# Performance work log

Hardware: AMD Instinct MI355X
Metric: run time of the kernel (lower is better)

Reference implementation:

```python
import math
import jax, jax.numpy as jnp
import numpy as np

B, S, D_MODEL, H = 8, 1024, 512, 8
HEAD = D_MODEL // H
MAX_REL = 16


def rel_index(length_q, length_k):
    # clipped relative-position index matrix [Lq, Lk] in [0, 2*MAX_REL]
    rq = jnp.arange(length_q)
    rk = jnp.arange(length_k)
    dist = rk[None, :] - rq[:, None]
    return jnp.clip(dist, -MAX_REL, MAX_REL) + MAX_REL


def setup_inputs() -> dict:
    key = jax.random.key(0)
    ks = jax.random.split(key, 13)
    sc = 1.0 / math.sqrt(D_MODEL)
    inp = {
        "query": jax.random.normal(ks[0], (B, S, D_MODEL), jnp.float32),
        "key": jax.random.normal(ks[1], (B, S, D_MODEL), jnp.float32),
        "value": jax.random.normal(ks[2], (B, S, D_MODEL), jnp.float32),
        "Wq": jax.random.normal(ks[3], (D_MODEL, D_MODEL), jnp.float32) * sc,
        "bq": jnp.zeros((D_MODEL,), jnp.float32),
        "Wk": jax.random.normal(ks[4], (D_MODEL, D_MODEL), jnp.float32) * sc,
        "bk": jnp.zeros((D_MODEL,), jnp.float32),
        "Wv": jax.random.normal(ks[5], (D_MODEL, D_MODEL), jnp.float32) * sc,
        "bv": jnp.zeros((D_MODEL,), jnp.float32),
        "Wo": jax.random.normal(ks[6], (D_MODEL, D_MODEL), jnp.float32) * sc,
        "bo": jnp.zeros((D_MODEL,), jnp.float32),
        "rel_k_table": jax.random.normal(ks[7], (2 * MAX_REL + 1, HEAD), jnp.float32),
        "rel_v_table": jax.random.normal(ks[8], (2 * MAX_REL + 1, HEAD), jnp.float32),
    }
    return inp


def reference(query, key, value, Wq, bq, Wk, bk, Wv, bv, Wo, bo, rel_k_table, rel_v_table):
    b, s, d = query.shape
    # input projections (torch Linear: x @ W.T + b)
    q = query @ Wq.T + bq  # [B,S,D]
    k = key @ Wk.T + bk
    v = value @ Wv.T + bv
    # split heads: [B,H,S,HEAD]
    qh = q.reshape(b, s, H, HEAD).transpose(0, 2, 1, 3)
    kh = k.reshape(b, s, H, HEAD).transpose(0, 2, 1, 3)
    vh = v.reshape(b, s, H, HEAD).transpose(0, 2, 1, 3)
    # content-content scores
    attn1 = jnp.einsum("bhqd,bhkd->bhqk", qh, kh)
    # content-position scores via gathered relative embeddings [S,S,HEAD]
    idx = rel_index(s, s)
    rk = rel_k_table[idx]
    attn2 = jnp.einsum("bhqd,qkd->bhqk", qh, rk)
    # NOTE: original code scales by sqrt(batch_size), reproduced faithfully
    scale = math.sqrt(float(B))
    attn = jax.nn.softmax((attn1 + attn2) / scale, axis=-1)
    # values: content + relative-position value term
    w1 = jnp.einsum("bhqk,bhkd->bhqd", attn, vh)
    rv = rel_v_table[idx]
    w2 = jnp.einsum("bhqk,qkd->bhqd", attn, rv)
    x = (w1 + w2).transpose(0, 2, 1, 3).reshape(b * s, d)
    return x @ Wo.T + bo
```

## Files before the change

kernel.cpp:

```cpp
#include <hip/hip_runtime.h>

typedef unsigned short u16;
typedef float f32x4 __attribute__((ext_vector_type(4)));
typedef __bf16 bf16x8 __attribute__((ext_vector_type(8)));

#define MFMA16(a, b, c) __builtin_amdgcn_mfma_f32_16x16x32_bf16((a), (b), (c), 0, 0, 0)

#define B_ 8
#define H_ 8
#define S_ 1024

__device__ __forceinline__ u16 f2bf(float f) {
  unsigned u = __float_as_uint(f);
  return (u16)((u + 0x7fffu + ((u >> 16) & 1u)) >> 16);
}
__device__ __forceinline__ unsigned cvtpk(float a, float b) {
  unsigned r;
  asm("v_cvt_pk_bf16_f32 %0, %1, %2" : "=v"(r) : "v"(a), "v"(b));
  return r;
}
__device__ __forceinline__ void gload16(const void* g, void* l) {
  __builtin_amdgcn_global_load_lds((__attribute__((address_space(1))) const void*)g,
                                   (__attribute__((address_space(3))) void*)l, 16, 0, 0);
}

__global__ void __launch_bounds__(256) convW(const float* __restrict__ s0, const float* __restrict__ s1,
                                             const float* __restrict__ s2, const float* __restrict__ s3,
                                             const float* __restrict__ s4,
                                             u16* __restrict__ d0, u16* __restrict__ d1, u16* __restrict__ d2,
                                             u16* __restrict__ d3, u16* __restrict__ d4) {
  size_t i = ((size_t)blockIdx.x * 256 + threadIdx.x) << 2;
  if (i >= 1050688) return;
  const float* s; u16* d; size_t off;
  if (i < 262144)       { s = s0; d = d0; off = i; }
  else if (i < 524288)  { s = s1; d = d1; off = i - 262144; }
  else if (i < 786432)  { s = s2; d = d2; off = i - 524288; }
  else if (i < 1048576) { s = s3; d = d3; off = i - 786432; }
  else                  { s = s4; d = d4; off = i - 1048576; }
  float4 f = *(const float4*)(s + off);
  uint2 o;
  o.x = cvtpk(f.x, f.y);
  o.y = cvtpk(f.z, f.w);
  *(uint2*)(d + off) = o;
}

__global__ void __launch_bounds__(512) qkv_gemm(const float* __restrict__ Aq, const float* __restrict__ Ak,
                                                const float* __restrict__ Av, const u16* __restrict__ Wqb,
                                                const u16* __restrict__ Wkb, const u16* __restrict__ Wvb,
                                                const float* __restrict__ bq, const float* __restrict__ bk,
                                                const float* __restrict__ bv, u16* __restrict__ Qh,
                                                u16* __restrict__ Kh, u16* __restrict__ Vt) {
  __shared__ float Asf[128 * 64];
  __shared__ u16 Bs[128 * 64];
  const int w = (blockIdx.x & 7) * 96 + (blockIdx.x >> 3);
  const int seg = w >> 8, bid = w & 255;
  const float* Af = seg == 0 ? Aq : (seg == 1 ? Ak : Av);
  const u16* W = seg == 0 ? Wqb : (seg == 1 ? Wkb : Wvb);
  const float* bias = seg == 0 ? bq : (seg == 1 ? bk : bv);
  const int tid = threadIdx.x, lane = tid & 63, wid = tid >> 6;
  const int c = lane & 15, g = lane >> 4;
  const int bm = bid >> 2, bn = bid & 3;
  const int m0 = bm << 7, n0 = bn << 7;
  const int wrow = (wid & 3) << 5;
  const int wcol = (wid >> 2) << 6;

  const f32x4 ZF = {0.f, 0.f, 0.f, 0.f};
  f32x4 acc[2][4];
#pragma unroll
  for (int i = 0; i < 2; ++i)
#pragma unroll
    for (int j = 0; j < 4; ++j) acc[i][j] = ZF;

  for (int kt = 0; kt < 512; kt += 64) {
    __syncthreads();
#pragma unroll
    for (int j = 0; j < 4; ++j) {
      int s0 = ((wid << 2) | j) << 6;
      int s = s0 + lane;
      int row = s >> 4;
      int colb_s = ((s & 15) << 4) ^ ((row & 7) << 4);
      gload16((const char*)Af + (((size_t)(m0 + row)) << 11) + (kt << 2) + colb_s,
              (char*)Asf + (s0 << 4));
    }
#pragma unroll
    for (int j = 0; j < 2; ++j) {
      int s0 = ((wid << 1) | j) << 6;
      int s = s0 + lane;
      int row = s >> 3;
      int off = ((s & 7) << 4) ^ ((row & 7) << 4);
      gload16((const char*)W + ((((size_t)(n0 + row)) << 9) + kt) * 2 + off,
              (char*)Bs + (s0 << 4));
    }
    __syncthreads();
#pragma unroll
    for (int kk = 0; kk < 2; ++kk) {
      bf16x8 af[2], bfr[4];
#pragma unroll
      for (int rt = 0; rt < 2; ++rt) {
        int row = wrow + (rt << 4) + c;
        int swz = (row & 7) << 4;
        const char* pA = (const char*)Asf + row * 256;
        int bb = (kk << 7) + (g << 5);
        float4 f0 = *(const float4*)(pA + (bb ^ swz));
        float4 f1 = *(const float4*)(pA + ((bb + 16) ^ swz));
        uint4 aw;
        aw.x = cvtpk(f0.x, f0.y); aw.y = cvtpk(f0.z, f0.w);
        aw.z = cvtpk(f1.x, f1.y); aw.w = cvtpk(f1.z, f1.w);
        af[rt] = __builtin_bit_cast(bf16x8, aw);
      }
#pragma unroll
      for (int ct = 0; ct < 4; ++ct) {
        int row = wcol + (ct << 4) + c;
        bfr[ct] = *(const bf16x8*)((const char*)Bs + row * 128 + (((kk << 6) | (g << 4)) ^ ((row & 7) << 4)));
      }
#pragma unroll
      for (int rt = 0; rt < 2; ++rt)
#pragma unroll
        for (int ct = 0; ct < 4; ++ct) acc[rt][ct] = MFMA16(af[rt], bfr[ct], acc[rt][ct]);
    }
  }

#pragma unroll
  for (int rt = 0; rt < 2; ++rt)
#pragma unroll
    for (int ct = 0; ct < 4; ++ct) {
      int n = n0 + wcol + (ct << 4) + c;
      float bv2 = bias[n];
      if (seg == 2) {
        int b2 = m0 >> 10;
        int sbase = (m0 & 1023) + wrow + (rt << 4) + (g << 2);
        int h2 = n >> 6, d2 = n & 63;
        uint2 o;
        o.x = cvtpk(acc[rt][ct][0] + bv2, acc[rt][ct][1] + bv2);
        o.y = cvtpk(acc[rt][ct][2] + bv2, acc[rt][ct][3] + bv2);
        *(uint2*)(Vt + ((((size_t)((b2 << 3) + h2) << 6) + d2) << 10) + sbase) = o;
      } else {
        u16* out = seg == 0 ? Qh : Kh;
#pragma unroll
        for (int r = 0; r < 4; ++r) {
          int m = m0 + wrow + (rt << 4) + (g << 2) + r;
          int b = m >> 10, s = m & 1023, h = n >> 6, d = n & 63;
          out[(((((size_t)(b * H_ + h)) << 10) + s) << 6) + d] = f2bf(acc[rt][ct][r] + bv2);
        }
      }
    }
}

__global__ void __launch_bounds__(512) gemm_out(const u16* __restrict__ A, const u16* __restrict__ W,
                                                const float* __restrict__ bias, float* __restrict__ out) {
  __shared__ u16 As[128 * 64];
  __shared__ u16 Bs[128 * 64];
  const int wb = (blockIdx.x & 7) * 32 + (blockIdx.x >> 3);
  const int tid = threadIdx.x, lane = tid & 63, wid = tid >> 6;
  const int c = lane & 15, g = lane >> 4;
  const int bm = wb >> 2, bn = wb & 3;
  const int m0 = bm << 7, n0 = bn << 7;
  const int wrow = (wid & 3) << 5;
  const int wcol = (wid >> 2) << 6;

  const f32x4 ZF = {0.f, 0.f, 0.f, 0.f};
  f32x4 acc[2][4];
#pragma unroll
  for (int i = 0; i < 2; ++i)
#pragma unroll
    for (int j = 0; j < 4; ++j) acc[i][j] = ZF;

  for (int kt = 0; kt < 512; kt += 64) {
    __syncthreads();
#pragma unroll
    for (int j = 0; j < 2; ++j) {
      int s0 = ((wid << 1) | j) << 6;
      int s = s0 + lane;
      int row = s >> 3;
      int off = ((s & 7) << 4) ^ ((row & 7) << 4);
      gload16((const char*)A + ((((size_t)(m0 + row)) << 9) + kt) * 2 + off, (char*)As + (s0 << 4));
      gload16((const char*)W + ((((size_t)(n0 + row)) << 9) + kt) * 2 + off, (char*)Bs + (s0 << 4));
    }
    __syncthreads();
#pragma unroll
    for (int kk = 0; kk < 2; ++kk) {
      bf16x8 af[2], bfr[4];
#pragma unroll
      for (int rt = 0; rt < 2; ++rt) {
        int row = wrow + (rt << 4) + c;
        af[rt] = *(const bf16x8*)((const char*)As + row * 128 + (((kk << 6) | (g << 4)) ^ ((row & 7) << 4)));
      }
#pragma unroll
      for (int ct = 0; ct < 4; ++ct) {
        int row = wcol + (ct << 4) + c;
        bfr[ct] = *(const bf16x8*)((const char*)Bs + row * 128 + (((kk << 6) | (g << 4)) ^ ((row & 7) << 4)));
      }
#pragma unroll
      for (int rt = 0; rt < 2; ++rt)
#pragma unroll
        for (int ct = 0; ct < 4; ++ct) acc[rt][ct] = MFMA16(af[rt], bfr[ct], acc[rt][ct]);
    }
  }

#pragma unroll
  for (int rt = 0; rt < 2; ++rt)
#pragma unroll
    for (int ct = 0; ct < 4; ++ct) {
      int n = n0 + wcol + (ct << 4) + c;
      float bv = bias[n];
#pragma unroll
      for (int r = 0; r < 4; ++r) {
        int m = m0 + wrow + (rt << 4) + (g << 2) + r;
        out[(((size_t)m) << 9) + n] = acc[rt][ct][r] + bv;
      }
    }
}

__global__ void __launch_bounds__(512) flash_kernel(const u16* __restrict__ Qh, const u16* __restrict__ Kh,
                                                    const u16* __restrict__ Vt, const u16* __restrict__ relkb,
                                                    const float* __restrict__ relv, u16* __restrict__ Xout) {
  __shared__ u16 Ks[2][64 * 64];
  __shared__ u16 Vs[2][64 * 64];
  __shared__ u16 Ps[128 * 64];
  __shared__ float qrelS[128 * 34];
  __shared__ u16 Pband[128 * 32];
  __shared__ float rv32S[64];

  const int tid = threadIdx.x, lane = tid & 63, wid = tid >> 6;
  const int c = lane & 15, g = lane >> 4;
  const int swz = ((blockIdx.x & 7) << 6) | (blockIdx.x >> 3);
  const int bh = swz >> 3, qt = swz & 7;
  const int qbase = qt << 7;
  const size_t rowbase = ((size_t)bh) << 10;
  const int qloc = (wid << 4) + c;
  const float K1 = 0.51013619f;
  const float C0 = 24.0f;

  bf16x8 qa[2];
  {
    const u16* qptr = Qh + ((rowbase + qbase + qloc) << 6);
    qa[0] = *(const bf16x8*)(qptr + (g << 3));
    qa[1] = *(const bf16x8*)(qptr + 32 + (g << 3));
  }

#define STAGE(buf, kt_) do { \
    const int k64_ = (kt_) << 6; \
    int L_ = (wid << 10) + lane * 16; \
    int row_ = L_ >> 7; \
    int off_ = (L_ & 127) ^ ((row_ & 7) << 4); \
    gload16((const char*)Kh + ((rowbase + k64_ + row_) << 7) + off_, (char*)Ks[buf] + (wid << 10)); \
    gload16((const char*)Vt + ((((size_t)bh << 6) + row_) << 11) + (k64_ << 1) + off_, (char*)Vs[buf] + (wid << 10)); \
  } while (0)

  STAGE(0, 0);

  ((uint4*)Pband)[tid] = uint4{0, 0, 0, 0};
  if (tid < 64) rv32S[tid] = relv[2048 + tid];

  {
    const f32x4 ZF = {0.f, 0.f, 0.f, 0.f};
#pragma unroll
    for (int t = 0; t < 3; ++t) {
      int rr = t * 16 + c; if (rr > 32) rr = 32;
      f32x4 qr = ZF;
#pragma unroll
      for (int kk = 0; kk < 2; ++kk) {
        bf16x8 ar = *(const bf16x8*)(relkb + (rr << 6) + (kk << 5) + (g << 3));
        qr = MFMA16(ar, qa[kk], qr);
      }
#pragma unroll
      for (int j = 0; j < 4; ++j) {
        int r = t * 16 + (g << 2) + j;
        if (r < 33) qrelS[qloc * 34 + r] = qr[j] * K1 - C0;
      }
    }
  }
  __syncthreads();

  const float bias_lo = qrelS[qloc * 34 + 0];
  const float bias_hi = qrelS[qloc * 34 + 32];

  int koff[4][2], voff[4][2], poffw[4];
#pragma unroll
  for (int t = 0; t < 4; ++t) {
#pragma unroll
    for (int kk = 0; kk < 2; ++kk)
      koff[t][kk] = ((t << 4) + c) * 128 + ((((kk << 6) | (g << 4))) ^ ((c & 7) << 4));
#pragma unroll
    for (int h2 = 0; h2 < 2; ++h2)
      voff[t][h2] = ((t << 4) + c) * 128 + ((((h2 << 6) | (g << 4))) ^ ((c & 7) << 4));
    poffw[t] = qloc * 128 + (((t << 5) | (g << 3)) ^ ((c & 7) << 4));
  }
  const int pr0 = qloc * 128 + ((g << 4) ^ ((c & 7) << 4));
  const int pr1 = pr0 ^ 64;

  const f32x4 ZF = {0.f, 0.f, 0.f, 0.f};
  f32x4 acc[4] = {ZF, ZF, ZF, ZF};
  float lsum = 0.f, lowsum = 0.f, psum = 0.f;

  for (int kt = 0; kt < 16; ++kt) {
    const int cur = kt & 1;
    if (kt < 15) STAGE(cur ^ 1, kt + 1);

    f32x4 sa[4];
#pragma unroll
    for (int t = 0; t < 4; ++t) {
      sa[t] = ZF;
#pragma unroll
      for (int kk = 0; kk < 2; ++kk) {
        bf16x8 bk = *(const bf16x8*)((const char*)Ks + (cur << 13) + koff[t][kk]);
        sa[t] = MFMA16(bk, qa[kk], sa[t]);
      }
    }

    const int D0 = (kt << 6) - qbase;
    float p[4][4];
    if (D0 >= 192) {
      float s = 0.f;
#pragma unroll
      for (int t = 0; t < 4; ++t)
#pragma unroll
        for (int j = 0; j < 4; ++j) {
          float pe = __builtin_amdgcn_exp2f(fmaf(sa[t][j], K1, bias_hi));
          p[t][j] = pe; s += pe;
        }
      lsum += s;
    } else if (D0 <= -128) {
      float s = 0.f;
#pragma unroll
      for (int t = 0; t < 4; ++t)
#pragma unroll
        for (int j = 0; j < 4; ++j) {
          float pe = __builtin_amdgcn_exp2f(fmaf(sa[t][j], K1, bias_lo));
          p[t][j] = pe; s += pe;
        }
      lsum += s; lowsum += s;
    } else {
#pragma unroll
      for (int t = 0; t < 4; ++t)
#pragma unroll
        for (int j = 0; j < 4; ++j) {
          int dlt = D0 + (t << 4) + (g << 2) + j - qloc;
          int idx = dlt < -16 ? 0 : (dlt > 16 ? 32 : dlt + 16);
          float pe = __builtin_amdgcn_exp2f(fmaf(sa[t][j], K1, qrelS[qloc * 34 + idx]));
          p[t][j] = pe;
          lsum += pe;
          if (dlt <= -16) lowsum += pe;
          else if (dlt < 16) { psum += pe; Pband[(qloc << 5) + dlt + 16] = f2bf(pe); }
        }
    }

#pragma unroll
    for (int t = 0; t < 4; ++t) {
      uint2 pk;
      pk.x = cvtpk(p[t][0], p[t][1]);
      pk.y = cvtpk(p[t][2], p[t][3]);
      *(uint2*)((char*)Ps + poffw[t]) = pk;
    }
    bf16x8 pb0 = *(const bf16x8*)((const char*)Ps + pr0);
    bf16x8 pb1 = *(const bf16x8*)((const char*)Ps + pr1);
#pragma unroll
    for (int dt = 0; dt < 4; ++dt) {
      bf16x8 av0 = *(const bf16x8*)((const char*)Vs + (cur << 13) + voff[dt][0]);
      bf16x8 av1 = *(const bf16x8*)((const char*)Vs + (cur << 13) + voff[dt][1]);
      acc[dt] = MFMA16(av0, pb0, acc[dt]);
      acc[dt] = MFMA16(av1, pb1, acc[dt]);
    }
    __syncthreads();
  }

  lsum += __shfl_xor(lsum, 16);   lsum += __shfl_xor(lsum, 32);
  lowsum += __shfl_xor(lowsum, 16); lowsum += __shfl_xor(lowsum, 32);
  psum += __shfl_xor(psum, 16);   psum += __shfl_xor(psum, 32);
  const float inv = 1.f / lsum;
  const float hsum = lsum - lowsum - psum;

  if (g == 0) Pband[qloc << 5] = f2bf(lowsum);

  u16* rvT = (u16*)qrelS;
  for (int i = tid; i < 4096; i += 512) rvT[i] = f2bf(relv[((i & 31) << 6) + (i >> 5)]);
  __syncthreads();

  bf16x8 pb2 = *(const bf16x8*)((const u16*)Pband + (qloc << 5) + (g << 3));
#pragma unroll
  for (int dt = 0; dt < 4; ++dt) {
    bf16x8 av = *(const bf16x8*)(rvT + (((dt << 4) + c) << 5) + (g << 3));
    acc[dt] = MFMA16(av, pb2, acc[dt]);
  }

  const int b = bh >> 3, h = bh & 7;
  const int q = qbase + qloc;
  u16* xb = Xout + ((((size_t)b << 10) + q) << 9) + (h << 6);
#pragma unroll
  for (int dt = 0; dt < 4; ++dt) {
    int d0 = (dt << 4) + (g << 2);
    float v0 = (acc[dt][0] + hsum * rv32S[d0 + 0]) * inv;
    float v1 = (acc[dt][1] + hsum * rv32S[d0 + 1]) * inv;
    float v2 = (acc[dt][2] + hsum * rv32S[d0 + 2]) * inv;
    float v3 = (acc[dt][3] + hsum * rv32S[d0 + 3]) * inv;
    uint2 o;
    o.x = cvtpk(v0, v1);
    o.y = cvtpk(v2, v3);
    *(uint2*)(xb + d0) = o;
  }
#undef STAGE
}

extern "C" void kernel_launch(void* const* d_in, const int* in_sizes, int n_in,
                              void* d_out, int out_size, void* d_ws, size_t ws_size,
                              hipStream_t stream) {
  (void)in_sizes; (void)n_in; (void)out_size; (void)ws_size;
  const float* query = (const float*)d_in[0];
  const float* key   = (const float*)d_in[1];
  const float* value = (const float*)d_in[2];
  const float* Wq = (const float*)d_in[3];
  const float* bq = (const float*)d_in[4];
  const float* Wk = (const float*)d_in[5];
  const float* bk = (const float*)d_in[6];
  const float* Wv = (const float*)d_in[7];
  const float* bv = (const float*)d_in[8];
  const float* Wo = (const float*)d_in[9];
  const float* bo = (const float*)d_in[10];
  const float* relk = (const float*)d_in[11];
  const float* relv = (const float*)d_in[12];

  char* ws = (char*)d_ws;
  u16*   Wqb   = (u16*)(ws + 25165824);
  u16*   Wkb   = (u16*)(ws + 25690112);
  u16*   Wvb   = (u16*)(ws + 26214400);
  u16*   Wob   = (u16*)(ws + 26738688);
  u16*   relkb = (u16*)(ws + 27262976);
  u16*   Qh    = (u16*)(ws + 27271168);
  u16*   Kh    = (u16*)(ws + 35659776);
  u16*   Vt    = (u16*)(ws + 52436992);
  u16*   Xout  = (u16*)(ws + 70262784);

  convW<<<1027, 256, 0, stream>>>(Wq, Wk, Wv, Wo, relk, Wqb, Wkb, Wvb, Wob, relkb);
  qkv_gemm<<<768, 512, 0, stream>>>(query, key, value, Wqb, Wkb, Wvb, bq, bk, bv, Qh, Kh, Vt);
  flash_kernel<<<512, 512, 0, stream>>>(Qh, Kh, Vt, relkb, relv, Xout);
  gemm_out<<<256, 512, 0, stream>>>(Xout, Wob, bo, (float*)d_out);
}
```

Measured before the change: 86.34 us.

## Double-buffer LDS staging in QKV and output projection GEMMs

Both projection GEMMs change from single-buffered 64-wide K tiles to double-buffered 32-wide K tiles. The next tile's global-to-LDS load is issued before the MFMAs on the current tile, so each iteration needs only one barrier. The aim is to hide global load latency behind compute. In exchange there are twice as many iterations and barriers, the swizzle is narrower (4-way on B), and LDS use stays the same.

```diff
diff --git a/kernel.cpp b/kernel.cpp
--- a/kernel.cpp
+++ b/kernel.cpp
@@ -50,8 +50,8 @@
                                                 const float* __restrict__ bq, const float* __restrict__ bk,
                                                 const float* __restrict__ bv, u16* __restrict__ Qh,
                                                 u16* __restrict__ Kh, u16* __restrict__ Vt) {
-  __shared__ float Asf[128 * 64];
-  __shared__ u16 Bs[128 * 64];
+  __shared__ float Asf[2][128 * 32];
+  __shared__ u16 Bs[2][128 * 32];
   const int w = (blockIdx.x & 7) * 96 + (blockIdx.x >> 3);
   const int seg = w >> 8, bid = w & 255;
   const float* Af = seg == 0 ? Aq : (seg == 1 ? Ak : Av);
@@ -64,6 +64,26 @@
   const int wrow = (wid & 3) << 5;
   const int wcol = (wid >> 2) << 6;
 
+#define STAGEQ(buf, kt_) do { \
+    _Pragma("unroll") \
+    for (int j_ = 0; j_ < 2; ++j_) { \
+      int s0_ = ((wid << 1) | j_) << 6; \
+      int s_ = s0_ + lane; \
+      int row_ = s_ >> 3; \
+      int sl_ = (s_ & 7) ^ (row_ & 7); \
+      gload16((const char*)Af + ((((size_t)(m0 + row_)) << 9) + (kt_)) * 4 + (sl_ << 4), \
+              (char*)Asf[buf] + (s0_ << 4)); \
+    } \
+    { \
+      int s0_ = wid << 6; \
+      int s_ = s0_ + lane; \
+      int row_ = s_ >> 2; \
+      int sl_ = (s_ & 3) ^ (row_ & 3); \
+      gload16((const char*)W + ((((size_t)(n0 + row_)) << 9) + (kt_)) * 2 + (sl_ << 4), \
+              (char*)Bs[buf] + (s0_ << 4)); \
+    } \
+  } while (0)
+
   const f32x4 ZF = {0.f, 0.f, 0.f, 0.f};
   f32x4 acc[2][4];
 #pragma unroll
@@ -71,53 +91,37 @@
 #pragma unroll
     for (int j = 0; j < 4; ++j) acc[i][j] = ZF;
 
-  for (int kt = 0; kt < 512; kt += 64) {
-    __syncthreads();
-#pragma unroll
-    for (int j = 0; j < 4; ++j) {
-      int s0 = ((wid << 2) | j) << 6;
-      int s = s0 + lane;
-      int row = s >> 4;
-      int colb_s = ((s & 15) << 4) ^ ((row & 7) << 4);
-      gload16((const char*)Af + (((size_t)(m0 + row)) << 11) + (kt << 2) + colb_s,
-              (char*)Asf + (s0 << 4));
-    }
-#pragma unroll
-    for (int j = 0; j < 2; ++j) {
-      int s0 = ((wid << 1) | j) << 6;
-      int s = s0 + lane;
-      int row = s >> 3;
-      int off = ((s & 7) << 4) ^ ((row & 7) << 4);
-      gload16((const char*)W + ((((size_t)(n0 + row)) << 9) + kt) * 2 + off,
-              (char*)Bs + (s0 << 4));
-    }
-    __syncthreads();
-#pragma unroll
-    for (int kk = 0; kk < 2; ++kk) {
-      bf16x8 af[2], bfr[4];
-#pragma unroll
-      for (int rt = 0; rt < 2; ++rt) {
-        int row = wrow + (rt << 4) + c;
-        int swz = (row & 7) << 4;
-        const char* pA = (const char*)Asf + row * 256;
-        int bb = (kk << 7) + (g << 5);
-        float4 f0 = *(const float4*)(pA + (bb ^ swz));
-        float4 f1 = *(const float4*)(pA + ((bb + 16) ^ swz));
-        uint4 aw;
-        aw.x = cvtpk(f0.x, f0.y); aw.y = cvtpk(f0.z, f0.w);
-        aw.z = cvtpk(f1.x, f1.y); aw.w = cvtpk(f1.z, f1.w);
-        af[rt] = __builtin_bit_cast(bf16x8, aw);
-      }
-#pragma unroll
-      for (int ct = 0; ct < 4; ++ct) {
-        int row = wcol + (ct << 4) + c;
-        bfr[ct] = *(const bf16x8*)((const char*)Bs + row * 128 + (((kk << 6) | (g << 4)) ^ ((row & 7) << 4)));
-      }
-#pragma unroll
-      for (int rt = 0; rt < 2; ++rt)
-#pragma unroll
-        for (int ct = 0; ct < 4; ++ct) acc[rt][ct] = MFMA16(af[rt], bfr[ct], acc[rt][ct]);
-    }
+  STAGEQ(0, 0);
+  __syncthreads();
+
+  for (int it = 0; it < 16; ++it) {
+    const int cur = it & 1;
+    if (it < 15) STAGEQ(cur ^ 1, (it + 1) << 5);
+
+    bf16x8 af[2], bfr[4];
+#pragma unroll
+    for (int rt = 0; rt < 2; ++rt) {
+      int row = wrow + (rt << 4) + c;
+      const char* pA = (const char*)Asf[cur] + row * 128;
+      int sw = row & 7;
+      float4 f0 = *(const float4*)(pA + ((((g << 1) | 0) ^ sw) << 4));
+      float4 f1 = *(const float4*)(pA + ((((g << 1) | 1) ^ sw) << 4));
+      uint4 aw;
+      aw.x = cvtpk(f0.x, f0.y); aw.y = cvtpk(f0.z, f0.w);
+      aw.z = cvtpk(f1.x, f1.y); aw.w = cvtpk(f1.z, f1.w);
+      af[rt] = __builtin_bit_cast(bf16x8, aw);
+    }
+#pragma unroll
+    for (int ct = 0; ct < 4; ++ct) {
+      int row = wcol + (ct << 4) + c;
+      bfr[ct] = *(const bf16x8*)((const char*)Bs[cur] + row * 64 + ((g ^ (row & 3)) << 4));
+    }
+#pragma unroll
+    for (int rt = 0; rt < 2; ++rt)
+#pragma unroll
+      for (int ct = 0; ct < 4; ++ct) acc[rt][ct] = MFMA16(af[rt], bfr[ct], acc[rt][ct]);
+
+    if (it < 15) __syncthreads();
   }
 
 #pragma unroll
@@ -144,12 +148,13 @@
         }
       }
     }
+#undef STAGEQ
 }
 
 __global__ void __launch_bounds__(512) gemm_out(const u16* __restrict__ A, const u16* __restrict__ W,
                                                 const float* __restrict__ bias, float* __restrict__ out) {
-  __shared__ u16 As[128 * 64];
-  __shared__ u16 Bs[128 * 64];
+  __shared__ u16 As2[2][128 * 32];
+  __shared__ u16 Bs2[2][128 * 32];
   const int wb = (blockIdx.x & 7) * 32 + (blockIdx.x >> 3);
   const int tid = threadIdx.x, lane = tid & 63, wid = tid >> 6;
   const int c = lane & 15, g = lane >> 4;
@@ -158,6 +163,17 @@
   const int wrow = (wid & 3) << 5;
   const int wcol = (wid >> 2) << 6;
 
+#define STAGEO(buf, kt_) do { \
+    int s0_ = wid << 6; \
+    int s_ = s0_ + lane; \
+    int row_ = s_ >> 2; \
+    int sl_ = (s_ & 3) ^ (row_ & 3); \
+    gload16((const char*)A + ((((size_t)(m0 + row_)) << 9) + (kt_)) * 2 + (sl_ << 4), \
+            (char*)As2[buf] + (s0_ << 4)); \
+    gload16((const char*)W + ((((size_t)(n0 + row_)) << 9) + (kt_)) * 2 + (sl_ << 4), \
+            (char*)Bs2[buf] + (s0_ << 4)); \
+  } while (0)
+
   const f32x4 ZF = {0.f, 0.f, 0.f, 0.f};
   f32x4 acc[2][4];
 #pragma unroll
@@ -165,36 +181,30 @@
 #pragma unroll
     for (int j = 0; j < 4; ++j) acc[i][j] = ZF;
 
-  for (int kt = 0; kt < 512; kt += 64) {
-    __syncthreads();
-#pragma unroll
-    for (int j = 0; j < 2; ++j) {
-      int s0 = ((wid << 1) | j) << 6;
-      int s = s0 + lane;
-      int row = s >> 3;
-      int off = ((s & 7) << 4) ^ ((row & 7) << 4);
-      gload16((const char*)A + ((((size_t)(m0 + row)) << 9) + kt) * 2 + off, (char*)As + (s0 << 4));
-      gload16((const char*)W + ((((size_t)(n0 + row)) << 9) + kt) * 2 + off, (char*)Bs + (s0 << 4));
-    }
-    __syncthreads();
-#pragma unroll
-    for (int kk = 0; kk < 2; ++kk) {
-      bf16x8 af[2], bfr[4];
-#pragma unroll
-      for (int rt = 0; rt < 2; ++rt) {
-        int row = wrow + (rt << 4) + c;
-        af[rt] = *(const bf16x8*)((const char*)As + row * 128 + (((kk << 6) | (g << 4)) ^ ((row & 7) << 4)));
-      }
-#pragma unroll
-      for (int ct = 0; ct < 4; ++ct) {
-        int row = wcol + (ct << 4) + c;
-        bfr[ct] = *(const bf16x8*)((const char*)Bs + row * 128 + (((kk << 6) | (g << 4)) ^ ((row & 7) << 4)));
-      }
-#pragma unroll
-      for (int rt = 0; rt < 2; ++rt)
-#pragma unroll
-        for (int ct = 0; ct < 4; ++ct) acc[rt][ct] = MFMA16(af[rt], bfr[ct], acc[rt][ct]);
-    }
+  STAGEO(0, 0);
+  __syncthreads();
+
+  for (int it = 0; it < 16; ++it) {
+    const int cur = it & 1;
+    if (it < 15) STAGEO(cur ^ 1, (it + 1) << 5);
+
+    bf16x8 af[2], bfr[4];
+#pragma unroll
+    for (int rt = 0; rt < 2; ++rt) {
+      int row = wrow + (rt << 4) + c;
+      af[rt] = *(const bf16x8*)((const char*)As2[cur] + row * 64 + ((g ^ (row & 3)) << 4));
+    }
+#pragma unroll
+    for (int ct = 0; ct < 4; ++ct) {
+      int row = wcol + (ct << 4) + c;
+      bfr[ct] = *(const bf16x8*)((const char*)Bs2[cur] + row * 64 + ((g ^ (row & 3)) << 4));
+    }
+#pragma unroll
+    for (int rt = 0; rt < 2; ++rt)
+#pragma unroll
+      for (int ct = 0; ct < 4; ++ct) acc[rt][ct] = MFMA16(af[rt], bfr[ct], acc[rt][ct]);
+
+    if (it < 15) __syncthreads();
   }
 
 #pragma unroll
@@ -209,6 +219,7 @@
         out[(((size_t)m) << 9) + n] = acc[rt][ct][r] + bv;
       }
     }
+#undef STAGEO
 }
 
 __global__ void __launch_bounds__(512) flash_kernel(const u16* __restrict__ Qh, const u16* __restrict__ Kh,
```

After: 86.02 us. About the same (-0.4%).
